# Optimization experiments

Hardware: AMD Instinct MI355X
Metric: run time of the kernel (lower is better)

Reference implementation:

```python
import jax, jax.numpy as jnp
import numpy as np
from jax import lax

B, CIN, COUT, H, W, K = 8, 64, 64, 96, 96, 3
PAD = K // 2
EPS = 1e-5


def _conv(x, w, pad):
    return lax.conv_general_dilated(x, w, window_strides=(1, 1),
                                    padding=[(pad, pad), (pad, pad)],
                                    dimension_numbers=('NCHW', 'OIHW', 'NCHW'))


def setup_inputs() -> dict:
    key = jax.random.key(0)
    ks = jax.random.split(key, 7)
    x = jax.random.normal(ks[0], (B, CIN, H, W), dtype=jnp.float32)
    # offset conv (zero-init in the original; use small random weights so offsets are nontrivial)
    w_off = jax.random.normal(ks[1], (2 * K * K, CIN, K, K), dtype=jnp.float32) * 0.01
    b_off = jax.random.normal(ks[2], (2 * K * K,), dtype=jnp.float32) * 0.01
    w_def = jax.random.normal(ks[3], (COUT, CIN, K, K), dtype=jnp.float32) * (1.0 / np.sqrt(CIN * K * K))
    b_def = jax.random.normal(ks[4], (COUT,), dtype=jnp.float32) * 0.01
    gamma = jax.random.normal(ks[5], (COUT,), dtype=jnp.float32) * 0.1 + 1.0
    beta = jax.random.normal(ks[6], (COUT,), dtype=jnp.float32) * 0.1
    return {"x": x, "w_off": w_off, "b_off": b_off, "w_def": w_def,
            "b_def": b_def, "gamma": gamma, "beta": beta}


def _deform_block(x, w_off, b_off, w_def, b_def, gamma, beta):
    # 1) predict offsets: [B, 2*K*K, H, W]; channel 2k = dy, 2k+1 = dx for tap k=ky*K+kx
    offset = _conv(x, w_off, PAD) + b_off[None, :, None, None]
    dy = offset[:, 0::2]  # [B, K*K, H, W]
    dx = offset[:, 1::2]

    # 2) sampling positions p = p0 + p_k + dp (stride 1, zero-padding semantics)
    yy = jnp.arange(H, dtype=jnp.float32)[:, None]          # [H,1]
    xx = jnp.arange(W, dtype=jnp.float32)[None, :]          # [1,W]
    kk = jnp.arange(K * K)
    ky = (kk // K - PAD).astype(jnp.float32)[None, :, None, None]
    kx = (kk % K - PAD).astype(jnp.float32)[None, :, None, None]
    py = yy[None, None] + ky + dy                            # [B, K*K, H, W]
    px = xx[None, None] + kx + dx

    # 3) bilinear gather with zero outside-boundary
    y0 = jnp.floor(py); x0 = jnp.floor(px)
    ly = py - y0; lx = px - x0
    x_flat = x.reshape(B, CIN, H * W)
    sampled = jnp.zeros((B, CIN, K * K, H, W), dtype=x.dtype)
    for iy, wy in ((y0, 1.0 - ly), (y0 + 1.0, ly)):
        for ix, wx in ((x0, 1.0 - lx), (x0 + 1.0, lx)):
            valid = (iy >= 0) & (iy < H) & (ix >= 0) & (ix < W)
            yi = jnp.clip(iy, 0, H - 1).astype(jnp.int32)
            xi = jnp.clip(ix, 0, W - 1).astype(jnp.int32)
            idx = (yi * W + xi).reshape(B, -1)               # [B, K*K*H*W]
            vals = jnp.take_along_axis(x_flat, idx[:, None, :], axis=2)
            vals = vals.reshape(B, CIN, K * K, H, W)
            wgt = (wy * wx * valid.astype(x.dtype))[:, None]  # [B,1,K*K,H,W]
            sampled = sampled + vals * wgt

    # 4) deformable conv = contraction of sampled taps with kernel weights
    out = jnp.einsum('bckhw,ock->bohw', sampled, w_def.reshape(COUT, CIN, K * K))
    out = out + b_def[None, :, None, None]

    # 5) BatchNorm (training-mode batch statistics) + ReLU
    mean = jnp.mean(out, axis=(0, 2, 3))
    var = jnp.var(out, axis=(0, 2, 3))
    out = (out - mean[None, :, None, None]) * lax.rsqrt(var + EPS)[None, :, None, None]
    out = out * gamma[None, :, None, None] + beta[None, :, None, None]
    return jax.nn.relu(out)


def reference(x, w_off, b_off, w_def, b_def, gamma, beta):
    return _deform_block(x, w_off, b_off, w_def, b_def, gamma, beta)
```

## Files before the change

### kernel.cpp

```cpp
#include <hip/hip_runtime.h>

#define Hh 96
#define Ww 96
#define CIN 64
#define COUT 64
#define BATCH 8
#define HW 9216
#define NOFF 18

#define XS_ROW   13824
#define XS_SIZE  124416
#define OF_BASE  124416
#define SM_TOTAL 135936

typedef __attribute__((ext_vector_type(8))) short bf16x8;
typedef __attribute__((ext_vector_type(4))) float f32x4;
typedef __attribute__((ext_vector_type(2))) float f32x2;

__device__ inline ushort f2bf(float f) {
  union { float f; uint u; } v; v.f = f;
  uint u = v.u;
  u += 0x7FFF + ((u >> 16) & 1);
  return (ushort)(u >> 16);
}
__device__ inline float bf2f(ushort s) {
  union { uint u; float f; } v; v.u = ((uint)s) << 16; return v.f;
}
__device__ inline uint cvtpk(float lo, float hi) {
  uint r;
  asm("v_cvt_pk_bf16_f32 %0, %1, %2" : "=v"(r) : "v"(lo), "v"(hi));
  return r;
}
__device__ inline f32x2 unpack2(uint u) {
  union { uint u[2]; f32x2 f; } r;
  r.u[0] = u << 16; r.u[1] = u & 0xFFFF0000u;
  return r.f;
}
__device__ inline f32x2 pkfma(f32x2 a, f32x2 b, f32x2 c) {
  f32x2 d;
  asm("v_pk_fma_f32 %0, %1, %2, %3" : "=v"(d) : "v"(a), "v"(b), "v"(c));
  return d;
}
__device__ inline f32x2 pkmul(f32x2 a, f32x2 b) {
  f32x2 d;
  asm("v_pk_mul_f32 %0, %1, %2" : "=v"(d) : "v"(a), "v"(b));
  return d;
}

__global__ __launch_bounds__(256) void k_wpack(
    const float* __restrict__ w_def, const float* __restrict__ w_off,
    ushort* __restrict__ wtb, ushort* __restrict__ wob)
{
  int g = blockIdx.x * 256 + threadIdx.x;
  if (g < 36864) {
    int k = g >> 12, o = (g >> 6) & 63, c = g & 63;
    wtb[g] = f2bf(w_def[(o * 64 + c) * 9 + k]);
  }
  int g2 = g - 36864;
  if (g2 >= 0 && g2 < 18432) {
    int k = g2 >> 11, n = (g2 >> 6) & 31, c = g2 & 63;
    wob[g2] = (n < NOFF) ? f2bf(w_off[(n * 64 + c) * 9 + k]) : (ushort)0;
  }
}

__global__ __launch_bounds__(768, 3) void k_main(
    const float* __restrict__ x, const ushort* __restrict__ wtb,
    const ushort* __restrict__ wob, const float* __restrict__ b_off,
    const float* __restrict__ b_def, float* __restrict__ out,
    float* __restrict__ parts)
{
  extern __shared__ char sm[];
  int tid = threadIdx.x;
  int bid = blockIdx.x;
  int b = bid & 7;
  int rt = bid >> 3;
  int r0 = rt * 3;

  {
    const float* xb_g = x + (size_t)b * CIN * HW;
    int px = tid >> 3, cg = tid & 7;
    #pragma unroll
    for (int s = 0; s < 9; ++s) {
      int srow = min(max(r0 - 3 + s, 0), 95);
      const float* src = xb_g + (size_t)(cg * 8) * HW + srow * 96 + px;
      float v[8];
      #pragma unroll
      for (int j = 0; j < 8; ++j) v[j] = src[(size_t)j * HW];
      uint u[4];
      u[0] = cvtpk(v[0], v[1]); u[1] = cvtpk(v[2], v[3]);
      u[2] = cvtpk(v[4], v[5]); u[3] = cvtpk(v[6], v[7]);
      *(uint4*)(sm + s * XS_ROW + px * 144 + cg * 16) = *(uint4*)u;
    }
  }
  __syncthreads();

  int wave = tid >> 6, lane = tid & 63;
  int m = lane & 15, hi = lane >> 4;
  int kh = wave & 1;
  int gb = wave >> 1;
  int khB = kh * 64, hiB = hi * 16;
  int chE = kh * 32 + hi * 8;

  int hA[3], wAc[3], pPix[3], gV[3];
  #pragma unroll
  for (int ti = 0; ti < 3; ++ti) {
    int g = gb + ti * 6;
    gV[ti] = g;
    int gr = g / 6, gc = g - gr * 6;
    hA[ti] = r0 + gr;
    wAc[ti] = gc * 16 + m;
    pPix[ti] = g * 16 + m;
  }

  f32x4 oacc[3][2];
  #pragma unroll
  for (int ti = 0; ti < 3; ++ti) {
    oacc[ti][0] = (f32x4){0.f, 0.f, 0.f, 0.f};
    oacc[ti][1] = (f32x4){0.f, 0.f, 0.f, 0.f};
  }
  for (int k = 0; k < 9; ++k) {
    int ky = k / 3 - 1, kx = (k - (k / 3) * 3) - 1;
    const ushort* wk = wob + k * 2048 + chE;
    bf16x8 wb0 = *(const bf16x8*)(wk + m * 64);
    bf16x8 wb1 = *(const bf16x8*)(wk + (16 + m) * 64);
    #pragma unroll
    for (int ti = 0; ti < 3; ++ti) {
      int yy = hA[ti] + ky, xx = wAc[ti] + kx;
      bool valid = (yy >= 0 && yy < Hh && xx >= 0 && xx < Ww);
      int cy = min(max(yy, 0), 95), cx = min(max(xx, 0), 95);
      int sy = cy - r0 + 3;
      bf16x8 a = *(const bf16x8*)(sm + sy * XS_ROW + cx * 144 + hiB + khB);
      if (!valid) a = (bf16x8)0;
      oacc[ti][0] = __builtin_amdgcn_mfma_f32_16x16x32_bf16(a, wb0, oacc[ti][0], 0, 0, 0);
      oacc[ti][1] = __builtin_amdgcn_mfma_f32_16x16x32_bf16(a, wb1, oacc[ti][1], 0, 0, 0);
    }
  }

  int j0 = m, j1 = 16 + m;
  if (kh == 1) {
    #pragma unroll
    for (int ti = 0; ti < 3; ++ti) {
      #pragma unroll
      for (int r = 0; r < 4; ++r) {
        int p = gV[ti] * 16 + hi * 4 + r;
        *(ushort*)(sm + OF_BASE + p * 40 + j0 * 2) = f2bf(oacc[ti][0][r]);
        if (m < 2)
          *(ushort*)(sm + OF_BASE + p * 40 + j1 * 2) = f2bf(oacc[ti][1][r]);
      }
    }
  }
  __syncthreads();
  if (kh == 0) {
    float bo0 = b_off[j0];
    float bo1 = (m < 2) ? b_off[j1] : 0.f;
    #pragma unroll
    for (int ti = 0; ti < 3; ++ti) {
      #pragma unroll
      for (int r = 0; r < 4; ++r) {
        int p = gV[ti] * 16 + hi * 4 + r;
        ushort* a0p = (ushort*)(sm + OF_BASE + p * 40 + j0 * 2);
        *a0p = f2bf(oacc[ti][0][r] + bf2f(*a0p) + bo0);
        if (m < 2) {
          ushort* a1p = (ushort*)(sm + OF_BASE + p * 40 + j1 * 2);
          *a1p = f2bf(oacc[ti][1][r] + bf2f(*a1p) + bo1);
        }
      }
    }
  }
  __syncthreads();

  f32x4 acc[3][4];
  #pragma unroll
  for (int ti = 0; ti < 3; ++ti)
    #pragma unroll
    for (int nt = 0; nt < 4; ++nt) acc[ti][nt] = (f32x4){0.f, 0.f, 0.f, 0.f};

  for (int k = 0; k < 9; ++k) {
    int ky = k / 3 - 1, kx = (k - (k / 3) * 3) - 1;
    const ushort* wk = wtb + k * 4096 + chE;
    bf16x8 bf0 = *(const bf16x8*)(wk + m * 64);
    bf16x8 bf1 = *(const bf16x8*)(wk + (16 + m) * 64);
    bf16x8 bf2 = *(const bf16x8*)(wk + (32 + m) * 64);
    bf16x8 bf3 = *(const bf16x8*)(wk + (48 + m) * 64);

    #pragma unroll
    for (int ti = 0; ti < 3; ++ti) {
      uint dd = *(const uint*)(sm + OF_BASE + pPix[ti] * 40 + k * 4);
      f32x2 dpair = unpack2(dd);
      float py = (float)(hA[ti] + ky) + dpair.x;
      float px = (float)(wAc[ti] + kx) + dpair.y;
      float y0f = floorf(py), x0f = floorf(px);
      float ly = py - y0f, lx = px - x0f;
      int y0 = (int)y0f, x0 = (int)x0f;
      int y1 = y0 + 1, x1 = x0 + 1;
      float fy0 = (y0 >= 0 && y0 < Hh) ? 1.f : 0.f;
      float fy1 = (y1 >= 0 && y1 < Hh) ? 1.f : 0.f;
      float fx0 = (x0 >= 0 && x0 < Ww) ? 1.f : 0.f;
      float fx1 = (x1 >= 0 && x1 < Ww) ? 1.f : 0.f;
      int cy0 = min(max(y0, 0), 95), cy1 = min(max(y1, 0), 95);
      int cx0 = min(max(x0, 0), 95), cx1 = min(max(x1, 0), 95);
      int sy0 = min(max(cy0 - r0 + 3, 0), 8);
      int sy1 = min(max(cy1 - r0 + 3, 0), 8);
      const char* row0 = sm + sy0 * XS_ROW;
      const char* row1 = sm + sy1 * XS_ROW;
      uint4 c00 = *(const uint4*)(row0 + cx0 * 144 + hiB + khB);
      uint4 c01 = *(const uint4*)(row0 + cx1 * 144 + hiB + khB);
      uint4 c10 = *(const uint4*)(row1 + cx0 * 144 + hiB + khB);
      uint4 c11 = *(const uint4*)(row1 + cx1 * 144 + hiB + khB);
      float s00 = (1.f - ly) * (1.f - lx) * (fy0 * fx0);
      float s01 = (1.f - ly) * lx * (fy0 * fx1);
      float s10 = ly * (1.f - lx) * (fy1 * fx0);
      float s11 = ly * lx * (fy1 * fx1);
      f32x2 w00 = (f32x2){s00, s00}, w01 = (f32x2){s01, s01};
      f32x2 w10 = (f32x2){s10, s10}, w11 = (f32x2){s11, s11};
      uint ua[4];
      {
        const uint* p00 = (const uint*)&c00; const uint* p01 = (const uint*)&c01;
        const uint* p10 = (const uint*)&c10; const uint* p11 = (const uint*)&c11;
        #pragma unroll
        for (int q = 0; q < 4; ++q) {
          f32x2 sv = pkmul(w00, unpack2(p00[q]));
          sv = pkfma(w01, unpack2(p01[q]), sv);
          sv = pkfma(w10, unpack2(p10[q]), sv);
          sv = pkfma(w11, unpack2(p11[q]), sv);
          ua[q] = cvtpk(sv.x, sv.y);
        }
      }
      bf16x8 av;
      __builtin_memcpy(&av, ua, 16);
      acc[ti][0] = __builtin_amdgcn_mfma_f32_16x16x32_bf16(av, bf0, acc[ti][0], 0, 0, 0);
      acc[ti][1] = __builtin_amdgcn_mfma_f32_16x16x32_bf16(av, bf1, acc[ti][1], 0, 0, 0);
      acc[ti][2] = __builtin_amdgcn_mfma_f32_16x16x32_bf16(av, bf2, acc[ti][2], 0, 0, 0);
      acc[ti][3] = __builtin_amdgcn_mfma_f32_16x16x32_bf16(av, bf3, acc[ti][3], 0, 0, 0);
    }
  }
  __syncthreads();

  float* T = (float*)sm;
  if (kh == 1) {
    #pragma unroll
    for (int ti = 0; ti < 3; ++ti)
      #pragma unroll
      for (int nt = 0; nt < 4; ++nt) {
        int o = nt * 16 + m;
        #pragma unroll
        for (int r = 0; r < 4; ++r) {
          int p = gV[ti] * 16 + hi * 4 + r;
          T[o * 289 + p] = acc[ti][nt][r];
        }
      }
  }
  __syncthreads();
  if (kh == 0) {
    float bd[4];
    bd[0] = b_def[m]; bd[1] = b_def[16 + m];
    bd[2] = b_def[32 + m]; bd[3] = b_def[48 + m];
    #pragma unroll
    for (int ti = 0; ti < 3; ++ti)
      #pragma unroll
      for (int nt = 0; nt < 4; ++nt) {
        int o = nt * 16 + m;
        #pragma unroll
        for (int r = 0; r < 4; ++r) {
          int p = gV[ti] * 16 + hi * 4 + r;
          T[o * 289 + p] += acc[ti][nt][r] + bd[nt];
        }
      }
  }
  __syncthreads();
  if (tid < 512) {
    int o = tid >> 3, seg = tid & 7;
    const float* Tr = T + o * 289 + seg * 36;
    float* og = out + ((size_t)(b * 64 + o)) * HW + rt * 288 + seg * 36;
    float s = 0.f, ss = 0.f;
    #pragma unroll
    for (int j4 = 0; j4 < 9; ++j4) {
      float4 v;
      v.x = Tr[j4 * 4 + 0]; v.y = Tr[j4 * 4 + 1];
      v.z = Tr[j4 * 4 + 2]; v.w = Tr[j4 * 4 + 3];
      s += v.x + v.y + v.z + v.w;
      ss += v.x * v.x + v.y * v.y + v.z * v.z + v.w * v.w;
      *(float4*)(og + j4 * 4) = v;
    }
    s += __shfl_down(s, 4); s += __shfl_down(s, 2); s += __shfl_down(s, 1);
    ss += __shfl_down(ss, 4); ss += __shfl_down(ss, 2); ss += __shfl_down(ss, 1);
    if ((tid & 7) == 0) {
      parts[o * 256 + bid] = s;
      parts[16384 + o * 256 + bid] = ss;
    }
  }
}

__global__ __launch_bounds__(256) void k_stats(
    const float* __restrict__ parts, const float* __restrict__ gamma,
    const float* __restrict__ beta, float* __restrict__ stats)
{
  int c = blockIdx.x;
  int tid = threadIdx.x;
  float s = 0.f, ss = 0.f;
  if (tid < 256) {
    s = parts[c * 256 + tid];
    ss = parts[16384 + c * 256 + tid];
  }
  #pragma unroll
  for (int off = 32; off >= 1; off >>= 1) {
    s += __shfl_down(s, off);
    ss += __shfl_down(ss, off);
  }
  __shared__ float rs[4], rss[4];
  int wave = tid >> 6, lane = tid & 63;
  if (lane == 0) { rs[wave] = s; rss[wave] = ss; }
  __syncthreads();
  if (tid == 0) {
    float S1 = rs[0] + rs[1] + rs[2] + rs[3];
    float S2 = rss[0] + rss[1] + rss[2] + rss[3];
    const float inv = 1.f / 73728.f;
    float mean = S1 * inv;
    float var = S2 * inv - mean * mean;
    float scale = gamma[c] * rsqrtf(var + 1e-5f);
    stats[c] = scale;
    stats[64 + c] = beta[c] - mean * scale;
  }
}

__global__ __launch_bounds__(256) void k_norm(
    float* __restrict__ out, const float* __restrict__ stats)
{
  int g = blockIdx.x * 256 + threadIdx.x;
  int o = (g / 2304) & 63;
  float sc = stats[o], sh = stats[64 + o];
  float4 v = ((const float4*)out)[g];
  v.x = fmaxf(fmaf(v.x, sc, sh), 0.f);
  v.y = fmaxf(fmaf(v.y, sc, sh), 0.f);
  v.z = fmaxf(fmaf(v.z, sc, sh), 0.f);
  v.w = fmaxf(fmaf(v.w, sc, sh), 0.f);
  ((float4*)out)[g] = v;
}

extern "C" void kernel_launch(void* const* d_in, const int* in_sizes, int n_in,
                              void* d_out, int out_size, void* d_ws, size_t ws_size,
                              hipStream_t stream) {
  const float* x     = (const float*)d_in[0];
  const float* w_off = (const float*)d_in[1];
  const float* b_off = (const float*)d_in[2];
  const float* w_def = (const float*)d_in[3];
  const float* b_def = (const float*)d_in[4];
  const float* gamma = (const float*)d_in[5];
  const float* beta  = (const float*)d_in[6];
  float* out = (float*)d_out;

  float* base  = (float*)d_ws;
  ushort* wtb  = (ushort*)base;
  ushort* wob  = (ushort*)(base + 18432);
  float* parts = base + 18432 + 9216;
  float* stats = parts + 32768;

  (void)hipFuncSetAttribute((const void*)k_main,
      hipFuncAttributeMaxDynamicSharedMemorySize, SM_TOTAL);

  k_wpack<<<216, 256, 0, stream>>>(w_def, w_off, wtb, wob);
  k_main<<<256, 768, SM_TOTAL, stream>>>(x, wtb, wob, b_off, b_def, out, parts);
  k_stats<<<64, 256, 0, stream>>>(parts, gamma, beta, stats);
  k_norm<<<4608, 256, 0, stream>>>(out, stats);
}
```

Before: 70.66 us.

## Pre-transpose input to bf16 NHWC and tile main kernel into 3x32 blocks

```diff
diff --git a/kernel.cpp b/kernel.cpp
--- a/kernel.cpp
+++ b/kernel.cpp
@@ -8,10 +8,11 @@
 #define HW 9216
 #define NOFF 18
 
-#define XS_ROW   13824
-#define XS_SIZE  124416
-#define OF_BASE  124416
-#define SM_TOTAL 135936
+#define XS_ROW   5472
+#define XS_SIZE  49248
+#define WS_BASE  49248
+#define OF_BASE  132192
+#define SM_TOTAL 136032
 
 typedef __attribute__((ext_vector_type(8))) short bf16x8;
 typedef __attribute__((ext_vector_type(4))) float f32x4;
@@ -63,8 +64,32 @@
   }
 }
 
+__global__ __launch_bounds__(256) void k_xt(
+    const float* __restrict__ x, ushort* __restrict__ xt)
+{
+  __shared__ float tile[64][65];
+  int tid = threadIdx.x;
+  int blk = blockIdx.x;
+  int b = blk / 144;
+  int pbase = (blk - b * 144) * 64;
+  int wave = tid >> 6, lane = tid & 63;
+  const float* xp = x + (size_t)b * CIN * HW + pbase;
+  #pragma unroll
+  for (int i = 0; i < 16; ++i) {
+    int c = wave * 16 + i;
+    tile[lane][c] = xp[(size_t)c * HW + lane];
+  }
+  __syncthreads();
+  ushort* xo = xt + ((size_t)b * HW + pbase) * 64;
+  #pragma unroll
+  for (int i = 0; i < 16; ++i) {
+    int p = wave * 16 + i;
+    xo[(size_t)p * 64 + lane] = f2bf(tile[p][lane]);
+  }
+}
+
 __global__ __launch_bounds__(768, 3) void k_main(
-    const float* __restrict__ x, const ushort* __restrict__ wtb,
+    const ushort* __restrict__ xt, const ushort* __restrict__ wtb,
     const ushort* __restrict__ wob, const float* __restrict__ b_off,
     const float* __restrict__ b_def, float* __restrict__ out,
     float* __restrict__ parts)
@@ -73,80 +98,70 @@
   int tid = threadIdx.x;
   int bid = blockIdx.x;
   int b = bid & 7;
-  int rt = bid >> 3;
-  int r0 = rt * 3;
+  int tile = bid >> 3;
+  int rt = tile / 3, cs = tile - rt * 3;
+  int r0 = rt * 3, c0 = cs * 32;
 
   {
-    const float* xb_g = x + (size_t)b * CIN * HW;
-    int px = tid >> 3, cg = tid & 7;
-    #pragma unroll
-    for (int s = 0; s < 9; ++s) {
+    const ushort* xsrc = xt + (size_t)b * HW * 64;
+    for (int q = tid; q < 2736; q += 768) {
+      int s = q / 304;
+      int rem = q - s * 304;
+      int cl = rem >> 3, cg = rem & 7;
       int srow = min(max(r0 - 3 + s, 0), 95);
-      const float* src = xb_g + (size_t)(cg * 8) * HW + srow * 96 + px;
-      float v[8];
-      #pragma unroll
-      for (int j = 0; j < 8; ++j) v[j] = src[(size_t)j * HW];
-      uint u[4];
-      u[0] = cvtpk(v[0], v[1]); u[1] = cvtpk(v[2], v[3]);
-      u[2] = cvtpk(v[4], v[5]); u[3] = cvtpk(v[6], v[7]);
-      *(uint4*)(sm + s * XS_ROW + px * 144 + cg * 16) = *(uint4*)u;
-    }
+      int scol = min(max(c0 - 3 + cl, 0), 95);
+      uint4 v = *(const uint4*)(xsrc + (size_t)(srow * 96 + scol) * 64 + cg * 8);
+      *(uint4*)(sm + s * XS_ROW + cl * 144 + cg * 16) = v;
+    }
+  }
+  for (int q = tid; q < 1296; q += 768) {
+    int k = q / 144;
+    int rem = q - k * 144;
+    int n = rem >> 3, cg = rem & 7;
+    uint4 v = *(const uint4*)(wob + k * 2048 + n * 64 + cg * 8);
+    *(uint4*)(sm + WS_BASE + k * 2592 + n * 144 + cg * 16) = v;
   }
   __syncthreads();
 
   int wave = tid >> 6, lane = tid & 63;
   int m = lane & 15, hi = lane >> 4;
   int kh = wave & 1;
-  int gb = wave >> 1;
+  int pg = wave >> 1;
   int khB = kh * 64, hiB = hi * 16;
-  int chE = kh * 32 + hi * 8;
-
-  int hA[3], wAc[3], pPix[3], gV[3];
-  #pragma unroll
-  for (int ti = 0; ti < 3; ++ti) {
-    int g = gb + ti * 6;
-    gV[ti] = g;
-    int gr = g / 6, gc = g - gr * 6;
-    hA[ti] = r0 + gr;
-    wAc[ti] = gc * 16 + m;
-    pPix[ti] = g * 16 + m;
-  }
-
-  f32x4 oacc[3][2];
-  #pragma unroll
-  for (int ti = 0; ti < 3; ++ti) {
-    oacc[ti][0] = (f32x4){0.f, 0.f, 0.f, 0.f};
-    oacc[ti][1] = (f32x4){0.f, 0.f, 0.f, 0.f};
-  }
-  for (int k = 0; k < 9; ++k) {
-    int ky = k / 3 - 1, kx = (k - (k / 3) * 3) - 1;
-    const ushort* wk = wob + k * 2048 + chE;
-    bf16x8 wb0 = *(const bf16x8*)(wk + m * 64);
-    bf16x8 wb1 = *(const bf16x8*)(wk + (16 + m) * 64);
-    #pragma unroll
-    for (int ti = 0; ti < 3; ++ti) {
-      int yy = hA[ti] + ky, xx = wAc[ti] + kx;
+
+  int hA = r0 + (pg >> 1);
+  int wA = c0 + (pg & 1) * 16 + m;
+  int p_pix = pg * 16 + m;
+
+  f32x4 oacc0 = (f32x4){0.f, 0.f, 0.f, 0.f};
+  f32x4 oacc1 = (f32x4){0.f, 0.f, 0.f, 0.f};
+  {
+    int r1 = min(16 + m, 17);
+    #pragma unroll
+    for (int k = 0; k < 9; ++k) {
+      int ky = k / 3 - 1, kx = (k - (k / 3) * 3) - 1;
+      const char* wkb = sm + WS_BASE + k * 2592;
+      bf16x8 wb0 = *(const bf16x8*)(wkb + m * 144 + hiB + khB);
+      bf16x8 wb1 = *(const bf16x8*)(wkb + r1 * 144 + hiB + khB);
+      int yy = hA + ky, xx = wA + kx;
       bool valid = (yy >= 0 && yy < Hh && xx >= 0 && xx < Ww);
-      int cy = min(max(yy, 0), 95), cx = min(max(xx, 0), 95);
-      int sy = cy - r0 + 3;
-      bf16x8 a = *(const bf16x8*)(sm + sy * XS_ROW + cx * 144 + hiB + khB);
+      int sy = min(max(yy, 0), 95) - r0 + 3;
+      int sx = min(max(xx, 0), 95) - c0 + 3;
+      bf16x8 a = *(const bf16x8*)(sm + sy * XS_ROW + sx * 144 + hiB + khB);
       if (!valid) a = (bf16x8)0;
-      oacc[ti][0] = __builtin_amdgcn_mfma_f32_16x16x32_bf16(a, wb0, oacc[ti][0], 0, 0, 0);
-      oacc[ti][1] = __builtin_amdgcn_mfma_f32_16x16x32_bf16(a, wb1, oacc[ti][1], 0, 0, 0);
+      oacc0 = __builtin_amdgcn_mfma_f32_16x16x32_bf16(a, wb0, oacc0, 0, 0, 0);
+      oacc1 = __builtin_amdgcn_mfma_f32_16x16x32_bf16(a, wb1, oacc1, 0, 0, 0);
     }
   }
 
   int j0 = m, j1 = 16 + m;
   if (kh == 1) {
     #pragma unroll
-    for (int ti = 0; ti < 3; ++ti) {
-      #pragma unroll
-      for (int r = 0; r < 4; ++r) {
-        int p = gV[ti] * 16 + hi * 4 + r;
-        *(ushort*)(sm + OF_BASE + p * 40 + j0 * 2) = f2bf(oacc[ti][0][r]);
-        if (m < 2)
-          *(ushort*)(sm + OF_BASE + p * 40 + j1 * 2) = f2bf(oacc[ti][1][r]);
-      }
+    for (int r = 0; r < 4; ++r) {
+      int p = pg * 16 + hi * 4 + r;
+      *(ushort*)(sm + OF_BASE + p * 40 + j0 * 2) = f2bf(oacc0[r]);
+      if (m < 2)
+        *(ushort*)(sm + OF_BASE + p * 40 + j1 * 2) = f2bf(oacc1[r]);
     }
   }
   __syncthreads();
@@ -154,101 +169,101 @@
     float bo0 = b_off[j0];
     float bo1 = (m < 2) ? b_off[j1] : 0.f;
     #pragma unroll
-    for (int ti = 0; ti < 3; ++ti) {
-      #pragma unroll
-      for (int r = 0; r < 4; ++r) {
-        int p = gV[ti] * 16 + hi * 4 + r;
-        ushort* a0p = (ushort*)(sm + OF_BASE + p * 40 + j0 * 2);
-        *a0p = f2bf(oacc[ti][0][r] + bf2f(*a0p) + bo0);
-        if (m < 2) {
-          ushort* a1p = (ushort*)(sm + OF_BASE + p * 40 + j1 * 2);
-          *a1p = f2bf(oacc[ti][1][r] + bf2f(*a1p) + bo1);
-        }
+    for (int r = 0; r < 4; ++r) {
+      int p = pg * 16 + hi * 4 + r;
+      ushort* a0p = (ushort*)(sm + OF_BASE + p * 40 + j0 * 2);
+      *a0p = f2bf(oacc0[r] + bf2f(*a0p) + bo0);
+      if (m < 2) {
+        ushort* a1p = (ushort*)(sm + OF_BASE + p * 40 + j1 * 2);
+        *a1p = f2bf(oacc1[r] + bf2f(*a1p) + bo1);
       }
     }
   }
-  __syncthreads();
-
-  f32x4 acc[3][4];
-  #pragma unroll
-  for (int ti = 0; ti < 3; ++ti)
-    #pragma unroll
-    for (int nt = 0; nt < 4; ++nt) acc[ti][nt] = (f32x4){0.f, 0.f, 0.f, 0.f};
-
+  for (int q = tid; q < 4608; q += 768) {
+    int k = q / 512;
+    int rem = q - k * 512;
+    int o = rem >> 3, cg = rem & 7;
+    uint4 v = *(const uint4*)(wtb + k * 4096 + o * 64 + cg * 8);
+    *(uint4*)(sm + WS_BASE + k * 9216 + o * 144 + cg * 16) = v;
+  }
+  __syncthreads();
+
+  f32x4 acc[4];
+  #pragma unroll
+  for (int nt = 0; nt < 4; ++nt) acc[nt] = (f32x4){0.f, 0.f, 0.f, 0.f};
+
+  uint od[9];
+  #pragma unroll
+  for (int k = 0; k < 9; ++k)
+    od[k] = *(const uint*)(sm + OF_BASE + p_pix * 40 + k * 4);
+
+  #pragma unroll 3
   for (int k = 0; k < 9; ++k) {
     int ky = k / 3 - 1, kx = (k - (k / 3) * 3) - 1;
-    const ushort* wk = wtb + k * 4096 + chE;
-    bf16x8 bf0 = *(const bf16x8*)(wk + m * 64);
-    bf16x8 bf1 = *(const bf16x8*)(wk + (16 + m) * 64);
-    bf16x8 bf2 = *(const bf16x8*)(wk + (32 + m) * 64);
-    bf16x8 bf3 = *(const bf16x8*)(wk + (48 + m) * 64);
-
-    #pragma unroll
-    for (int ti = 0; ti < 3; ++ti) {
-      uint dd = *(const uint*)(sm + OF_BASE + pPix[ti] * 40 + k * 4);
-      f32x2 dpair = unpack2(dd);
-      float py = (float)(hA[ti] + ky) + dpair.x;
-      float px = (float)(wAc[ti] + kx) + dpair.y;
-      float y0f = floorf(py), x0f = floorf(px);
-      float ly = py - y0f, lx = px - x0f;
-      int y0 = (int)y0f, x0 = (int)x0f;
-      int y1 = y0 + 1, x1 = x0 + 1;
-      float fy0 = (y0 >= 0 && y0 < Hh) ? 1.f : 0.f;
-      float fy1 = (y1 >= 0 && y1 < Hh) ? 1.f : 0.f;
-      float fx0 = (x0 >= 0 && x0 < Ww) ? 1.f : 0.f;
-      float fx1 = (x1 >= 0 && x1 < Ww) ? 1.f : 0.f;
-      int cy0 = min(max(y0, 0), 95), cy1 = min(max(y1, 0), 95);
-      int cx0 = min(max(x0, 0), 95), cx1 = min(max(x1, 0), 95);
-      int sy0 = min(max(cy0 - r0 + 3, 0), 8);
-      int sy1 = min(max(cy1 - r0 + 3, 0), 8);
-      const char* row0 = sm + sy0 * XS_ROW;
-      const char* row1 = sm + sy1 * XS_ROW;
-      uint4 c00 = *(const uint4*)(row0 + cx0 * 144 + hiB + khB);
-      uint4 c01 = *(const uint4*)(row0 + cx1 * 144 + hiB + khB);
-      uint4 c10 = *(const uint4*)(row1 + cx0 * 144 + hiB + khB);
-      uint4 c11 = *(const uint4*)(row1 + cx1 * 144 + hiB + khB);
-      float s00 = (1.f - ly) * (1.f - lx) * (fy0 * fx0);
-      float s01 = (1.f - ly) * lx * (fy0 * fx1);
-      float s10 = ly * (1.f - lx) * (fy1 * fx0);
-      float s11 = ly * lx * (fy1 * fx1);
-      f32x2 w00 = (f32x2){s00, s00}, w01 = (f32x2){s01, s01};
-      f32x2 w10 = (f32x2){s10, s10}, w11 = (f32x2){s11, s11};
-      uint ua[4];
-      {
-        const uint* p00 = (const uint*)&c00; const uint* p01 = (const uint*)&c01;
-        const uint* p10 = (const uint*)&c10; const uint* p11 = (const uint*)&c11;
-        #pragma unroll
-        for (int q = 0; q < 4; ++q) {
-          f32x2 sv = pkmul(w00, unpack2(p00[q]));
-          sv = pkfma(w01, unpack2(p01[q]), sv);
-          sv = pkfma(w10, unpack2(p10[q]), sv);
-          sv = pkfma(w11, unpack2(p11[q]), sv);
-          ua[q] = cvtpk(sv.x, sv.y);
-        }
+    const char* wkb = sm + WS_BASE + k * 9216;
+    bf16x8 bf0 = *(const bf16x8*)(wkb + m * 144 + hiB + khB);
+    bf16x8 bf1 = *(const bf16x8*)(wkb + (16 + m) * 144 + hiB + khB);
+    bf16x8 bf2 = *(const bf16x8*)(wkb + (32 + m) * 144 + hiB + khB);
+    bf16x8 bf3 = *(const bf16x8*)(wkb + (48 + m) * 144 + hiB + khB);
+
+    f32x2 dpair = unpack2(od[k]);
+    float py = (float)(hA + ky) + dpair.x;
+    float px = (float)(wA + kx) + dpair.y;
+    float y0f = floorf(py), x0f = floorf(px);
+    float ly = py - y0f, lx = px - x0f;
+    int y0 = (int)y0f, x0 = (int)x0f;
+    int y1 = y0 + 1, x1 = x0 + 1;
+    float fy0 = (y0 >= 0 && y0 < Hh) ? 1.f : 0.f;
+    float fy1 = (y1 >= 0 && y1 < Hh) ? 1.f : 0.f;
+    float fx0 = (x0 >= 0 && x0 < Ww) ? 1.f : 0.f;
+    float fx1 = (x1 >= 0 && x1 < Ww) ? 1.f : 0.f;
+    int sy0 = min(max(min(max(y0, 0), 95) - r0 + 3, 0), 8);
+    int sy1 = min(max(min(max(y1, 0), 95) - r0 + 3, 0), 8);
+    int sx0 = min(max(min(max(x0, 0), 95) - c0 + 3, 0), 37);
+    int sx1 = min(max(min(max(x1, 0), 95) - c0 + 3, 0), 37);
+    const char* row0 = sm + sy0 * XS_ROW;
+    const char* row1 = sm + sy1 * XS_ROW;
+    uint4 c00 = *(const uint4*)(row0 + sx0 * 144 + hiB + khB);
+    uint4 c01 = *(const uint4*)(row0 + sx1 * 144 + hiB + khB);
+    uint4 c10 = *(const uint4*)(row1 + sx0 * 144 + hiB + khB);
+    uint4 c11 = *(const uint4*)(row1 + sx1 * 144 + hiB + khB);
+    float s00 = (1.f - ly) * (1.f - lx) * (fy0 * fx0);
+    float s01 = (1.f - ly) * lx * (fy0 * fx1);
+    float s10 = ly * (1.f - lx) * (fy1 * fx0);
+    float s11 = ly * lx * (fy1 * fx1);
+    f32x2 w00 = (f32x2){s00, s00}, w01 = (f32x2){s01, s01};
+    f32x2 w10 = (f32x2){s10, s10}, w11 = (f32x2){s11, s11};
+    uint ua[4];
+    {
+      const uint* p00 = (const uint*)&c00; const uint* p01 = (const uint*)&c01;
+      const uint* p10 = (const uint*)&c10; const uint* p11 = (const uint*)&c11;
+      #pragma unroll
+      for (int q = 0; q < 4; ++q) {
+        f32x2 sv = pkmul(w00, unpack2(p00[q]));
+        sv = pkfma(w01, unpack2(p01[q]), sv);
+        sv = pkfma(w10, unpack2(p10[q]), sv);
+        sv = pkfma(w11, unpack2(p11[q]), sv);
+        ua[q] = cvtpk(sv.x, sv.y);
       }
-      bf16x8 av;
-      __builtin_memcpy(&av, ua, 16);
-      acc[ti][0] = __builtin_amdgcn_mfma_f32_16x16x32_bf16(av, bf0, acc[ti][0], 0, 0, 0);
-      acc[ti][1] = __builtin_amdgcn_mfma_f32_16x16x32_bf16(av, bf1, acc[ti][1], 0, 0, 0);
-      acc[ti][2] = __builtin_amdgcn_mfma_f32_16x16x32_bf16(av, bf2, acc[ti][2], 0, 0, 0);
-      acc[ti][3] = __builtin_amdgcn_mfma_f32_16x16x32_bf16(av, bf3, acc[ti][3], 0, 0, 0);
-    }
+    }
+    bf16x8 av;
+    __builtin_memcpy(&av, ua, 16);
+    acc[0] = __builtin_amdgcn_mfma_f32_16x16x32_bf16(av, bf0, acc[0], 0, 0, 0);
+    acc[1] = __builtin_amdgcn_mfma_f32_16x16x32_bf16(av, bf1, acc[1], 0, 0, 0);
+    acc[2] = __builtin_amdgcn_mfma_f32_16x16x32_bf16(av, bf2, acc[2], 0, 0, 0);
+    acc[3] = __builtin_amdgcn_mfma_f32_16x16x32_bf16(av, bf3, acc[3], 0, 0, 0);
   }
   __syncthreads();
 
   float* T = (float*)sm;
   if (kh == 1) {
     #pragma unroll
-    for (int ti = 0; ti < 3; ++ti)
+    for (int nt = 0; nt < 4; ++nt) {
+      int o = nt * 16 + m;
       #pragma unroll
-      for (int nt = 0; nt < 4; ++nt) {
-        int o = nt * 16 + m;
-        #pragma unroll
-        for (int r = 0; r < 4; ++r) {
-          int p = gV[ti] * 16 + hi * 4 + r;
-          T[o * 289 + p] = acc[ti][nt][r];
-        }
-      }
+      for (int r = 0; r < 4; ++r)
+        T[o * 97 + pg * 16 + hi * 4 + r] = acc[nt][r];
+    }
   }
   __syncthreads();
   if (kh == 0) {
@@ -256,37 +271,36 @@
     bd[0] = b_def[m]; bd[1] = b_def[16 + m];
     bd[2] = b_def[32 + m]; bd[3] = b_def[48 + m];
     #pragma unroll
-    for (int ti = 0; ti < 3; ++ti)
+    for (int nt = 0; nt < 4; ++nt) {
+      int o = nt * 16 + m;
       #pragma unroll
-      for (int nt = 0; nt < 4; ++nt) {
-        int o = nt * 16 + m;
-        #pragma unroll
-        for (int r = 0; r < 4; ++r) {
-          int p = gV[ti] * 16 + hi * 4 + r;
-          T[o * 289 + p] += acc[ti][nt][r] + bd[nt];
-        }
+      for (int r = 0; r < 4; ++r) {
+        int p = pg * 16 + hi * 4 + r;
+        T[o * 97 + p] += acc[nt][r] + bd[nt];
       }
+    }
   }
   __syncthreads();
   if (tid < 512) {
     int o = tid >> 3, seg = tid & 7;
-    const float* Tr = T + o * 289 + seg * 36;
-    float* og = out + ((size_t)(b * 64 + o)) * HW + rt * 288 + seg * 36;
+    const float* Tr = T + o * 97 + seg * 12;
+    float* og = out + (size_t)(b * 64 + o) * HW;
     float s = 0.f, ss = 0.f;
     #pragma unroll
-    for (int j4 = 0; j4 < 9; ++j4) {
+    for (int j4 = 0; j4 < 3; ++j4) {
+      int px = seg * 12 + j4 * 4;
       float4 v;
       v.x = Tr[j4 * 4 + 0]; v.y = Tr[j4 * 4 + 1];
       v.z = Tr[j4 * 4 + 2]; v.w = Tr[j4 * 4 + 3];
       s += v.x + v.y + v.z + v.w;
       ss += v.x * v.x + v.y * v.y + v.z * v.z + v.w * v.w;
-      *(float4*)(og + j4 * 4) = v;
+      *(float4*)(og + (r0 + (px >> 5)) * 96 + c0 + (px & 31)) = v;
     }
     s += __shfl_down(s, 4); s += __shfl_down(s, 2); s += __shfl_down(s, 1);
     ss += __shfl_down(ss, 4); ss += __shfl_down(ss, 2); ss += __shfl_down(ss, 1);
     if ((tid & 7) == 0) {
-      parts[o * 256 + bid] = s;
-      parts[16384 + o * 256 + bid] = ss;
+      parts[o * 768 + bid] = s;
+      parts[49152 + o * 768 + bid] = ss;
     }
   }
 }
@@ -298,9 +312,9 @@
   int c = blockIdx.x;
   int tid = threadIdx.x;
   float s = 0.f, ss = 0.f;
-  if (tid < 256) {
-    s = parts[c * 256 + tid];
-    ss = parts[16384 + c * 256 + tid];
+  for (int i = tid; i < 768; i += 256) {
+    s += parts[c * 768 + i];
+    ss += parts[49152 + c * 768 + i];
   }
   #pragma unroll
   for (int off = 32; off >= 1; off >>= 1) {
@@ -352,14 +366,16 @@
   float* base  = (float*)d_ws;
   ushort* wtb  = (ushort*)base;
   ushort* wob  = (ushort*)(base + 18432);
-  float* parts = base + 18432 + 9216;
-  float* stats = parts + 32768;
+  ushort* xt   = (ushort*)(base + 18432 + 9216);
+  float* parts = base + 18432 + 9216 + 2359296;
+  float* stats = parts + 98304;
 
   (void)hipFuncSetAttribute((const void*)k_main,
       hipFuncAttributeMaxDynamicSharedMemorySize, SM_TOTAL);
 
   k_wpack<<<216, 256, 0, stream>>>(w_def, w_off, wtb, wob);
-  k_main<<<256, 768, SM_TOTAL, stream>>>(x, wtb, wob, b_off, b_def, out, parts);
+  k_xt<<<1152, 256, 0, stream>>>(x, xt);
+  k_main<<<768, 768, SM_TOTAL, stream>>>(xt, wtb, wob, b_off, b_def, out, parts);
   k_stats<<<64, 256, 0, stream>>>(parts, gamma, beta, stats);
   k_norm<<<4608, 256, 0, stream>>>(out, stats);
 }
```

New measurement: 69.77 us. About the same (-1.3%).
